# Performance work log

Measured on AMD Instinct MI355X. Metric: run time of the kernel, lower is better.

Reference implementation:

```python
import jax, jax.numpy as jnp
import numpy as np

B, S, E, H = 2, 2048, 2048, 16
D = E // H  # head_dim = 128
ROPE_BASE = 10000.0


def _rope_tables(seq_len, dim, dtype):
    inv_freq = 1.0 / (ROPE_BASE ** (jnp.arange(0, dim, 2, dtype=jnp.float32) / dim))
    pos = jnp.arange(seq_len, dtype=jnp.float32)
    freqs = jnp.outer(pos, inv_freq)            # [S, D/2]
    emb = jnp.concatenate([freqs, freqs], -1)    # [S, D]
    return jnp.cos(emb).astype(dtype), jnp.sin(emb).astype(dtype)


def _rotate_half(x):
    x1, x2 = jnp.split(x, 2, axis=-1)
    return jnp.concatenate([-x2, x1], axis=-1)


def _apply_rope(x, cos, sin):
    # x: [B,H,S,D]; cos/sin: [S,D] broadcast over batch+heads
    return x * cos[None, None] + _rotate_half(x) * sin[None, None]


def setup_inputs() -> dict:
    key = jax.random.key(0)
    k1, k2, k3 = jax.random.split(key, 3)
    x = jax.random.normal(k1, (B, S, E), dtype=jnp.float32)
    w_qkv = jax.random.normal(k2, (3 * E, E), dtype=jnp.float32) * (E ** -0.5)
    w_out = jax.random.normal(k3, (E, E), dtype=jnp.float32) * (E ** -0.5)
    return {"x": x, "w_qkv": w_qkv, "w_out": w_out}


def reference(x, w_qkv, w_out):
    b, s, e = x.shape
    qkv = x @ w_qkv.T                                # [B,S,3E]
    q, k, v = jnp.split(qkv, 3, axis=-1)
    def to_heads(t):
        return t.reshape(b, s, H, D).transpose(0, 2, 1, 3)  # [B,H,S,D]
    q, k, v = to_heads(q), to_heads(k), to_heads(v)
    cos, sin = _rope_tables(s, D, x.dtype)
    q = _apply_rope(q, cos, sin)
    k = _apply_rope(k, cos, sin)
    scale = 1.0 / jnp.sqrt(jnp.asarray(D, x.dtype))
    scores = jnp.einsum('bhqd,bhkd->bhqk', q, k) * scale
    causal = jnp.tril(jnp.ones((s, s), dtype=bool))
    scores = jnp.where(causal[None, None], scores, jnp.asarray(-jnp.inf, scores.dtype))
    attn = jax.nn.softmax(scores, axis=-1)
    y = jnp.einsum('bhqk,bhkd->bhqd', attn, v)       # [B,H,S,D]
    y = y.transpose(0, 2, 1, 3).reshape(b, s, e)
    return y @ w_out.T
```

## Files before the change

kernel.cpp:

```cpp
#include <hip/hip_runtime.h>
#include <stdint.h>

constexpr int BATCH = 2;
constexpr int SEQ   = 2048;
constexpr int EMB   = 2048;
constexpr int NH    = 16;
constexpr int HD    = 128;
constexpr int QKV3  = 3 * EMB;

typedef unsigned short u16;
typedef __attribute__((ext_vector_type(8))) short bf16x8;
typedef __attribute__((ext_vector_type(4))) float floatx4;

__device__ inline float bf2f(u16 u) {
  union { unsigned int i; float f; } v; v.i = ((unsigned int)u) << 16; return v.f;
}
__device__ inline u16 f2bf(float f) {
  union { float f; unsigned int i; } v; v.f = f;
  unsigned int x = v.i;
  return (u16)((x + 0x7fffu + ((x >> 16) & 1u)) >> 16);
}

__device__ inline void load_lds16(const void* g, void* l) {
  __builtin_amdgcn_global_load_lds((const __attribute__((address_space(1))) unsigned int*)g,
                                   (__attribute__((address_space(3))) unsigned int*)l,
                                   16, 0, 0);
}

__device__ inline void block_barrier() {
  __builtin_amdgcn_sched_barrier(0);
  asm volatile("" ::: "memory");
  __builtin_amdgcn_s_barrier();
  asm volatile("" ::: "memory");
  __builtin_amdgcn_sched_barrier(0);
}

__global__ void cvt_f32_bf16(const float* __restrict__ src, u16* __restrict__ dst, int n4) {
  const int i = blockIdx.x * blockDim.x + threadIdx.x;
  if (i < n4) {
    const float4 v = ((const float4*)src)[i];
    ushort4 o;
    o.x = f2bf(v.x); o.y = f2bf(v.y); o.z = f2bf(v.z); o.w = f2bf(v.w);
    ((ushort4*)dst)[i] = o;
  }
}

__global__ __launch_bounds__(512, 2) void gemm_bt192(const u16* __restrict__ A,
                                                     const u16* __restrict__ Bm,
                                                     u16* __restrict__ Cb,
                                                     int M, int N, int K) {
  __shared__ __align__(16) u16 sh[57344];
  char* ldsb = (char*)sh;

  const int tid  = threadIdx.x;
  const int wave = tid >> 6, lane = tid & 63;
  const int wrow = wave >> 1;
  const int wcol = wave & 1;
  const int m0 = blockIdx.y * 256, n0 = blockIdx.x * 192;
  const int frow = lane & 15, quad = lane >> 4;
  const int KT = K >> 6;

  const int srow8 = tid >> 3;
  const int scolE = (((tid & 7) ^ (srow8 & 7)) << 3);
  auto stageT = [&](int t, int d) {
#pragma unroll
    for (int a = 0; a < 4; ++a) {
      const int r = a * 64 + srow8;
      load_lds16(A + (size_t)(m0 + r) * K + t * 64 + scolE,
                 ldsb + d * 57344 + a * 8192 + wave * 1024);
    }
#pragma unroll
    for (int bi = 0; bi < 3; ++bi) {
      const int r = bi * 64 + srow8;
      load_lds16(Bm + (size_t)(n0 + r) * K + t * 64 + scolE,
                 ldsb + d * 57344 + 32768 + bi * 8192 + wave * 1024);
    }
  };

  floatx4 acc[4][6];
#pragma unroll
  for (int i = 0; i < 4; ++i)
#pragma unroll
    for (int j = 0; j < 6; ++j) acc[i][j] = {0.f, 0.f, 0.f, 0.f};

  stageT(0, 0);

  for (int t = 0; t < KT; ++t) {
    const int d = t & 1, dn = d ^ 1;
    const char* dbuf = ldsb + d * 57344;

    block_barrier();
    if (t + 1 < KT) {
      stageT(t + 1, dn);
      asm volatile("s_waitcnt vmcnt(7)" ::: "memory");
    } else {
      asm volatile("s_waitcnt vmcnt(0)" ::: "memory");
    }
    block_barrier();

    bf16x8 af[4][2], bf0[2][2], bf1[2][2], bf2[2][2];
#pragma unroll
    for (int mi = 0; mi < 4; ++mi) {
      const int ra = wrow * 64 + mi * 16 + frow;
#pragma unroll
      for (int kk = 0; kk < 2; ++kk) {
        const int cb = (kk * 64 + quad * 16) ^ ((ra & 7) << 4);
        af[mi][kk] = *(const bf16x8*)(dbuf + ra * 128 + cb);
      }
    }
#pragma unroll
    for (int ni = 0; ni < 2; ++ni) {
      const int rb = wcol * 96 + ni * 16 + frow;
#pragma unroll
      for (int kk = 0; kk < 2; ++kk) {
        const int cb = (kk * 64 + quad * 16) ^ ((rb & 7) << 4);
        bf0[ni][kk] = *(const bf16x8*)(dbuf + 32768 + rb * 128 + cb);
      }
    }
#pragma unroll
    for (int ni = 0; ni < 2; ++ni) {
      const int rb = wcol * 96 + (2 + ni) * 16 + frow;
#pragma unroll
      for (int kk = 0; kk < 2; ++kk) {
        const int cb = (kk * 64 + quad * 16) ^ ((rb & 7) << 4);
        bf1[ni][kk] = *(const bf16x8*)(dbuf + 32768 + rb * 128 + cb);
      }
    }
    asm volatile("s_waitcnt lgkmcnt(4)" ::: "memory");
    __builtin_amdgcn_sched_barrier(0);
    __builtin_amdgcn_s_setprio(1);
#pragma unroll
    for (int mi = 0; mi < 4; ++mi)
#pragma unroll
      for (int ni = 0; ni < 2; ++ni)
#pragma unroll
        for (int kk = 0; kk < 2; ++kk)
          acc[mi][ni] = __builtin_amdgcn_mfma_f32_16x16x32_bf16(af[mi][kk], bf0[ni][kk], acc[mi][ni], 0, 0, 0);
    __builtin_amdgcn_s_setprio(0);

#pragma unroll
    for (int ni = 0; ni < 2; ++ni) {
      const int rb = wcol * 96 + (4 + ni) * 16 + frow;
#pragma unroll
      for (int kk = 0; kk < 2; ++kk) {
        const int cb = (kk * 64 + quad * 16) ^ ((rb & 7) << 4);
        bf2[ni][kk] = *(const bf16x8*)(dbuf + 32768 + rb * 128 + cb);
      }
    }
    asm volatile("s_waitcnt lgkmcnt(4)" ::: "memory");
    __builtin_amdgcn_sched_barrier(0);
    __builtin_amdgcn_s_setprio(1);
#pragma unroll
    for (int mi = 0; mi < 4; ++mi)
#pragma unroll
      for (int ni = 0; ni < 2; ++ni)
#pragma unroll
        for (int kk = 0; kk < 2; ++kk)
          acc[mi][2 + ni] = __builtin_amdgcn_mfma_f32_16x16x32_bf16(af[mi][kk], bf1[ni][kk], acc[mi][2 + ni], 0, 0, 0);
    __builtin_amdgcn_s_setprio(0);

    asm volatile("s_waitcnt lgkmcnt(0)" ::: "memory");
    __builtin_amdgcn_sched_barrier(0);
    __builtin_amdgcn_s_setprio(1);
#pragma unroll
    for (int mi = 0; mi < 4; ++mi)
#pragma unroll
      for (int ni = 0; ni < 2; ++ni)
#pragma unroll
        for (int kk = 0; kk < 2; ++kk)
          acc[mi][4 + ni] = __builtin_amdgcn_mfma_f32_16x16x32_bf16(af[mi][kk], bf2[ni][kk], acc[mi][4 + ni], 0, 0, 0);
    __builtin_amdgcn_s_setprio(0);
  }

#pragma unroll
  for (int mi = 0; mi < 4; ++mi)
#pragma unroll
    for (int ni = 0; ni < 6; ++ni) {
      const int row = m0 + wrow * 64 + mi * 16 + quad * 4;
      const int col = n0 + wcol * 96 + ni * 16 + frow;
#pragma unroll
      for (int r = 0; r < 4; ++r)
        Cb[(size_t)(row + r) * N + col] = f2bf(acc[mi][ni][r]);
    }
}

__global__ __launch_bounds__(512, 2) void gemm_bt128f(const u16* __restrict__ A,
                                                      const u16* __restrict__ Bm,
                                                      float* __restrict__ Cf,
                                                      int M, int N, int K) {
  __shared__ __align__(16) u16 sh[49152];
  char* ldsb = (char*)sh;

  const int tid  = threadIdx.x;
  const int wave = tid >> 6, lane = tid & 63;
  const int wrow = wave >> 1;
  const int wcol = wave & 1;
  const int m0 = blockIdx.y * 256, n0 = blockIdx.x * 128;
  const int frow = lane & 15, quad = lane >> 4;
  const int KT = K >> 6;

  const int srow8 = tid >> 3;
  const int scolE = (((tid & 7) ^ (srow8 & 7)) << 3);
  auto stageT = [&](int t, int d) {
#pragma unroll
    for (int a = 0; a < 4; ++a) {
      const int r = a * 64 + srow8;
      load_lds16(A + (size_t)(m0 + r) * K + t * 64 + scolE,
                 ldsb + d * 49152 + a * 8192 + wave * 1024);
    }
#pragma unroll
    for (int bi = 0; bi < 2; ++bi) {
      const int r = bi * 64 + srow8;
      load_lds16(Bm + (size_t)(n0 + r) * K + t * 64 + scolE,
                 ldsb + d * 49152 + 32768 + bi * 8192 + wave * 1024);
    }
  };

  floatx4 acc[4][4];
#pragma unroll
  for (int i = 0; i < 4; ++i)
#pragma unroll
    for (int j = 0; j < 4; ++j) acc[i][j] = {0.f, 0.f, 0.f, 0.f};

  stageT(0, 0);

  for (int t = 0; t < KT; ++t) {
    const int d = t & 1, dn = d ^ 1;
    const char* dbuf = ldsb + d * 49152;

    block_barrier();
    if (t + 1 < KT) {
      stageT(t + 1, dn);
      asm volatile("s_waitcnt vmcnt(6)" ::: "memory");
    } else {
      asm volatile("s_waitcnt vmcnt(0)" ::: "memory");
    }
    block_barrier();

    bf16x8 af[4][2], bf0[2][2], bf1[2][2];
#pragma unroll
    for (int mi = 0; mi < 4; ++mi) {
      const int ra = wrow * 64 + mi * 16 + frow;
#pragma unroll
      for (int kk = 0; kk < 2; ++kk) {
        const int cb = (kk * 64 + quad * 16) ^ ((ra & 7) << 4);
        af[mi][kk] = *(const bf16x8*)(dbuf + ra * 128 + cb);
      }
    }
#pragma unroll
    for (int ni = 0; ni < 2; ++ni) {
      const int rb = wcol * 64 + ni * 16 + frow;
#pragma unroll
      for (int kk = 0; kk < 2; ++kk) {
        const int cb = (kk * 64 + quad * 16) ^ ((rb & 7) << 4);
        bf0[ni][kk] = *(const bf16x8*)(dbuf + 32768 + rb * 128 + cb);
      }
    }
#pragma unroll
    for (int ni = 0; ni < 2; ++ni) {
      const int rb = wcol * 64 + (2 + ni) * 16 + frow;
#pragma unroll
      for (int kk = 0; kk < 2; ++kk) {
        const int cb = (kk * 64 + quad * 16) ^ ((rb & 7) << 4);
        bf1[ni][kk] = *(const bf16x8*)(dbuf + 32768 + rb * 128 + cb);
      }
    }
    asm volatile("s_waitcnt lgkmcnt(4)" ::: "memory");
    __builtin_amdgcn_sched_barrier(0);
    __builtin_amdgcn_s_setprio(1);
#pragma unroll
    for (int mi = 0; mi < 4; ++mi)
#pragma unroll
      for (int ni = 0; ni < 2; ++ni)
#pragma unroll
        for (int kk = 0; kk < 2; ++kk)
          acc[mi][ni] = __builtin_amdgcn_mfma_f32_16x16x32_bf16(af[mi][kk], bf0[ni][kk], acc[mi][ni], 0, 0, 0);
    __builtin_amdgcn_s_setprio(0);

    asm volatile("s_waitcnt lgkmcnt(0)" ::: "memory");
    __builtin_amdgcn_sched_barrier(0);
    __builtin_amdgcn_s_setprio(1);
#pragma unroll
    for (int mi = 0; mi < 4; ++mi)
#pragma unroll
      for (int ni = 0; ni < 2; ++ni)
#pragma unroll
        for (int kk = 0; kk < 2; ++kk)
          acc[mi][2 + ni] = __builtin_amdgcn_mfma_f32_16x16x32_bf16(af[mi][kk], bf1[ni][kk], acc[mi][2 + ni], 0, 0, 0);
    __builtin_amdgcn_s_setprio(0);
  }

#pragma unroll
  for (int mi = 0; mi < 4; ++mi)
#pragma unroll
    for (int ni = 0; ni < 4; ++ni) {
      const int row = m0 + wrow * 64 + mi * 16 + quad * 4;
      const int col = n0 + wcol * 64 + ni * 16 + frow;
#pragma unroll
      for (int r = 0; r < 4; ++r)
        Cf[(size_t)(row + r) * N + col] = acc[mi][ni][r];
    }
}

__global__ void rope_inplace(u16* __restrict__ qkv) {
  const int t   = blockIdx.x * blockDim.x + threadIdx.x;
  const int j   = t & 63;
  const int idx = t >> 6;
  const int h   = idx & (NH - 1);
  const int bs  = idx >> 4;
  const int s   = bs & (SEQ - 1);

  u16* base = qkv + (size_t)bs * QKV3 + h * HD;

  const float inv_freq = exp2f(-(float)j * (13.287712379549449f / 64.0f));
  const float ang = (float)s * inv_freq;
  const float c = cosf(ang), sn = sinf(ang);

#pragma unroll
  for (int part = 0; part < 2; ++part) {
    u16* p = base + part * EMB;
    const float x1 = bf2f(p[j]), x2 = bf2f(p[j + 64]);
    p[j]      = f2bf(x1 * c - x2 * sn);
    p[j + 64] = f2bf(x2 * c + x1 * sn);
  }
}

__global__ __launch_bounds__(256) void transpose_v(const u16* __restrict__ qkv,
                                                   u16* __restrict__ VT) {
  __shared__ u16 vtile[64][136];
  const int tid = threadIdx.x;
  const int s0 = blockIdx.x * 64;
  const int bh = blockIdx.y;
  const int b = bh >> 4, h = bh & 15;

  const u16* Vp = qkv + (size_t)b * SEQ * QKV3 + 2 * EMB + h * HD;
  {
    const int r = tid >> 2, cp = (tid & 3) * 32;
    const uint4* src = (const uint4*)(Vp + (size_t)(s0 + r) * QKV3 + cp);
    uint4* dst = (uint4*)&vtile[r][cp];
    dst[0] = src[0]; dst[1] = src[1]; dst[2] = src[2]; dst[3] = src[3];
  }
  __syncthreads();
  {
    const int d = tid >> 1, ck = (tid & 1) * 32;
    ushort4 o[8];
#pragma unroll
    for (int i = 0; i < 8; ++i) {
      o[i].x = vtile[ck + i * 4 + 0][d];
      o[i].y = vtile[ck + i * 4 + 1][d];
      o[i].z = vtile[ck + i * 4 + 2][d];
      o[i].w = vtile[ck + i * 4 + 3][d];
    }
    ushort4* dst = (ushort4*)(VT + ((size_t)bh * HD + d) * SEQ + s0 + ck);
#pragma unroll
    for (int i = 0; i < 8; ++i) dst[i] = o[i];
  }
}

constexpr int PSTR = 72;

__global__ __launch_bounds__(256, 2) void attn_mfma(const u16* __restrict__ qkv,
                                                    const u16* __restrict__ VT,
                                                    u16* __restrict__ Y) {
  __shared__ __align__(16) u16 kb[2][64 * 128];
  __shared__ __align__(16) u16 vb[2][64 * 128];
  __shared__ __align__(16) u16 p_sh[4][16][PSTR];

  const int tid  = threadIdx.x;
  const int wave = tid >> 6, lane = tid & 63;
  const int bid  = blockIdx.x;
  const int bh   = bid & 31;
  const int pc   = bid >> 5;
  const int cq   = (pc < 8) ? pc : 23 - pc;
  const int qa   = cq;
  const int qb   = 31 - cq;
  const int b = bh >> 4, h = bh & 15;

  const u16* Qp  = qkv + (size_t)b * SEQ * QKV3 + h * HD;
  const u16* Kp  = Qp + EMB;
  const u16* VTp = VT + (size_t)bh * HD * SEQ;

  const int NT = 32 - cq;

  u16* kbf = &kb[0][0];

  {
    const int rl  = lane >> 4;
    const int cbp = (lane & 15) * 16;
#pragma unroll
    for (int i = 0; i < 8; ++i) {
      const int cc = wave * 8 + i;
      const int r  = cc * 4 + rl;
      const int gq = (r < 64) ? (qa * 64 + r) : (qb * 64 + r - 64);
      const int cbl = cbp ^ ((r & 7) << 4);
      load_lds16(Qp + (size_t)gq * QKV3 + (cbl >> 1), kbf + cc * 512);
    }
  }
  asm volatile("s_waitcnt vmcnt(0)" ::: "memory");
  block_barrier();

  const int frow = lane & 15;
  const int quad = lane >> 4;

  bf16x8 aq[2][4];
#pragma unroll
  for (int m = 0; m < 2; ++m)
#pragma unroll
    for (int ks = 0; ks < 4; ++ks) {
      const int qr = m * 64 + wave * 16 + frow;
      const int cb = (ks * 64 + quad * 16) ^ ((qr & 7) << 4);
      aq[m][ks] = *(const bf16x8*)((const char*)kbf + qr * 256 + cb);
    }
  asm volatile("s_waitcnt lgkmcnt(0)" ::: "memory");
  block_barrier();

  auto stage_k = [&](int t, int sel) {
    const int rl  = lane >> 4;
    const int cbp = (lane & 15) * 16;
#pragma unroll
    for (int i = 0; i < 4; ++i) {
      const int cc = wave * 4 + i;
      const int r  = cc * 4 + rl;
      const int cbl = cbp ^ ((r & 7) << 4);
      load_lds16(Kp + (size_t)(t * 64 + r) * QKV3 + (cbl >> 1), &kb[sel][cc * 512]);
    }
  };
  auto stage_v = [&](int t, int sel) {
    const int rl  = lane >> 3;
    const int cbp = (lane & 7) * 16;
#pragma unroll
    for (int i = 0; i < 4; ++i) {
      const int cc = wave * 4 + i;
      const int r  = cc * 8 + rl;
      const int cbl = cbp ^ ((r & 7) << 4);
      load_lds16(VTp + (size_t)r * SEQ + t * 64 + (cbl >> 1), &vb[sel][cc * 512]);
    }
  };

  floatx4 o_acc[2][8];
#pragma unroll
  for (int m = 0; m < 2; ++m)
#pragma unroll
    for (int dt = 0; dt < 8; ++dt) o_acc[m][dt] = {0.f, 0.f, 0.f, 0.f};
  float l_r[2][4];
#pragma unroll
  for (int m = 0; m < 2; ++m)
#pragma unroll
    for (int r = 0; r < 4; ++r) l_r[m][r] = 0.f;

  const float scale = 0.08838834764831845f;
  const float M0s   = 3.5355339059327378f;

  stage_k(0, 0);
  stage_v(0, 0);

  for (int t = 0; t < NT; ++t) {
    block_barrier();
    const bool havek = (t + 1 < NT);
    if (havek) {
      stage_k(t + 1, (t + 1) & 1);
      stage_v(t + 1, (t + 1) & 1);
      asm volatile("s_waitcnt vmcnt(8)" ::: "memory");
    } else {
      asm volatile("s_waitcnt vmcnt(0)" ::: "memory");
    }
    block_barrier();

    const char* kbuf = (const char*)&kb[t & 1][0];
    const char* vbuf = (const char*)&vb[t & 1][0];
    const bool aAct = (t <= qa);

    floatx4 s4[2][4];
    __builtin_amdgcn_s_setprio(1);
    if (aAct) {
#pragma unroll
      for (int nt = 0; nt < 4; ++nt) {
        floatx4 a0 = {0.f, 0.f, 0.f, 0.f}, a1 = {0.f, 0.f, 0.f, 0.f};
#pragma unroll
        for (int ks = 0; ks < 4; ++ks) {
          const int kr = nt * 16 + frow;
          const int cb = (ks * 64 + quad * 16) ^ ((kr & 7) << 4);
          const bf16x8 bk = *(const bf16x8*)(kbuf + kr * 256 + cb);
          a0 = __builtin_amdgcn_mfma_f32_16x16x32_bf16(aq[0][ks], bk, a0, 0, 0, 0);
          a1 = __builtin_amdgcn_mfma_f32_16x16x32_bf16(aq[1][ks], bk, a1, 0, 0, 0);
        }
        s4[0][nt] = a0; s4[1][nt] = a1;
      }
    } else {
#pragma unroll
      for (int nt = 0; nt < 4; ++nt) {
        floatx4 a1 = {0.f, 0.f, 0.f, 0.f};
#pragma unroll
        for (int ks = 0; ks < 4; ++ks) {
          const int kr = nt * 16 + frow;
          const int cb = (ks * 64 + quad * 16) ^ ((kr & 7) << 4);
          const bf16x8 bk = *(const bf16x8*)(kbuf + kr * 256 + cb);
          a1 = __builtin_amdgcn_mfma_f32_16x16x32_bf16(aq[1][ks], bk, a1, 0, 0, 0);
        }
        s4[1][nt] = a1;
      }
    }
    __builtin_amdgcn_s_setprio(0);

#pragma unroll
    for (int m = 0; m < 2; ++m) {
      if (m == 0 && !aAct) continue;
      const int tdiag = (m == 0) ? qa : qb;
      if (t == tdiag) {
#pragma unroll
        for (int nt = 0; nt < 4; ++nt)
#pragma unroll
          for (int r = 0; r < 4; ++r) {
            const int key = t * 64 + nt * 16 + frow;
            const int qg  = tdiag * 64 + wave * 16 + quad * 4 + r;
            if (key > qg) s4[m][nt][r] = -1.0e30f;
          }
      }
#pragma unroll
      for (int nt = 0; nt < 4; ++nt)
#pragma unroll
        for (int r = 0; r < 4; ++r)
          s4[m][nt][r] = __expf(fmaf(s4[m][nt][r], scale, -M0s));
#pragma unroll
      for (int r = 0; r < 4; ++r)
        l_r[m][r] += (s4[m][0][r] + s4[m][1][r]) + (s4[m][2][r] + s4[m][3][r]);
    }

    __builtin_amdgcn_s_setprio(1);
#pragma unroll
    for (int m = 0; m < 2; ++m) {
      if (m == 0 && !aAct) continue;
#pragma unroll
      for (int nt = 0; nt < 4; ++nt)
#pragma unroll
        for (int r = 0; r < 4; ++r)
          p_sh[wave][quad * 4 + r][nt * 16 + frow] = f2bf(s4[m][nt][r]);
#pragma unroll
      for (int step = 0; step < 2; ++step) {
        const bf16x8 ap = *(const bf16x8*)&p_sh[wave][frow][step * 32 + quad * 8];
#pragma unroll
        for (int dt = 0; dt < 8; ++dt) {
          const int vr = dt * 16 + frow;
          const int cb = (step * 64 + quad * 16) ^ ((vr & 7) << 4);
          const bf16x8 bv = *(const bf16x8*)(vbuf + vr * 128 + cb);
          o_acc[m][dt] = __builtin_amdgcn_mfma_f32_16x16x32_bf16(ap, bv, o_acc[m][dt], 0, 0, 0);
        }
      }
    }
    __builtin_amdgcn_s_setprio(0);
  }

#pragma unroll
  for (int off = 1; off <= 8; off <<= 1)
#pragma unroll
    for (int m = 0; m < 2; ++m)
#pragma unroll
      for (int r = 0; r < 4; ++r) l_r[m][r] += __shfl_xor(l_r[m][r], off);

#pragma unroll
  for (int m = 0; m < 2; ++m) {
    const int qbase = ((m == 0) ? qa : qb) * 64 + wave * 16;
    float invl[4];
#pragma unroll
    for (int r = 0; r < 4; ++r) invl[r] = 1.f / l_r[m][r];
#pragma unroll
    for (int dt = 0; dt < 8; ++dt)
#pragma unroll
      for (int r = 0; r < 4; ++r) {
        const int qg = qbase + quad * 4 + r;
        const size_t off = ((size_t)b * SEQ + qg) * EMB + h * HD + dt * 16 + frow;
        Y[off] = f2bf(o_acc[m][dt][r] * invl[r]);
      }
  }
}

extern "C" void kernel_launch(void* const* d_in, const int* in_sizes, int n_in,
                              void* d_out, int out_size, void* d_ws, size_t ws_size,
                              hipStream_t stream) {
  const float* x_f     = (const float*)d_in[0];
  const float* w_qkv_f = (const float*)d_in[1];
  const float* w_out_f = (const float*)d_in[2];
  float* out = (float*)d_out;

  const int M = BATCH * SEQ;
  const size_t n_x    = (size_t)M * EMB;
  const size_t n_wqkv = (size_t)3 * EMB * EMB;
  const size_t n_wout = (size_t)EMB * EMB;

  u16* xb    = (u16*)d_ws;
  u16* wqkvb = xb + n_x;
  u16* qkv   = wqkvb + n_wqkv;
  u16* VT    = qkv + (size_t)M * QKV3;
  u16* woutb = wqkvb;
  u16* Yb    = xb;

  cvt_f32_bf16<<<(int)((n_x / 4 + 255) / 256), 256, 0, stream>>>(x_f, xb, (int)(n_x / 4));
  cvt_f32_bf16<<<(int)((n_wqkv / 4 + 255) / 256), 256, 0, stream>>>(w_qkv_f, wqkvb, (int)(n_wqkv / 4));

  gemm_bt192<<<dim3(QKV3 / 192, M / 256), 512, 0, stream>>>(
      xb, wqkvb, qkv, M, QKV3, EMB);

  rope_inplace<<<(BATCH * SEQ * NH * 64) / 256, 256, 0, stream>>>(qkv);
  transpose_v<<<dim3(SEQ / 64, BATCH * NH), 256, 0, stream>>>(qkv, VT);

  cvt_f32_bf16<<<(int)((n_wout / 4 + 255) / 256), 256, 0, stream>>>(w_out_f, woutb, (int)(n_wout / 4));

  attn_mfma<<<dim3((SEQ / 128) * BATCH * NH), 256, 0, stream>>>(qkv, VT, Yb);

  gemm_bt128f<<<dim3(EMB / 128, M / 256), 512, 0, stream>>>(
      Yb, woutb, out, M, EMB, EMB);
}
```

Baseline: 362.9 us.

## Interleave global-to-LDS prefetch chunks with MFMA phases in both GEMM kernels

Restructures the main loop of both GEMM kernels so the next tile's global-to-LDS loads are issued in small chunks spread across several MFMA phases, instead of all at once at the top of the iteration. The 192-wide kernel now computes in four 2x3 sub-block quadrants with extra block barriers between them. The goal is to spread memory traffic across the iteration and overlap it with compute. In exchange it adds many block barriers per iteration and a full vmcnt(0) wait at the top of each iteration, which could serialize the waves.

Measured after the change: 357.2 us. No clear change (-1.6%).

```diff
diff --git a/kernel.cpp b/kernel.cpp
--- a/kernel.cpp
+++ b/kernel.cpp
@@ -62,15 +62,13 @@
 
   const int srow8 = tid >> 3;
   const int scolE = (((tid & 7) ^ (srow8 & 7)) << 3);
-  auto stageT = [&](int t, int d) {
-#pragma unroll
-    for (int a = 0; a < 4; ++a) {
-      const int r = a * 64 + srow8;
+  auto stage1 = [&](int t, int d, int j) {
+    if (j < 4) {
+      const int r = j * 64 + srow8;
       load_lds16(A + (size_t)(m0 + r) * K + t * 64 + scolE,
-                 ldsb + d * 57344 + a * 8192 + wave * 1024);
-    }
-#pragma unroll
-    for (int bi = 0; bi < 3; ++bi) {
+                 ldsb + d * 57344 + j * 8192 + wave * 1024);
+    } else {
+      const int bi = j - 4;
       const int r = bi * 64 + srow8;
       load_lds16(Bm + (size_t)(n0 + r) * K + t * 64 + scolE,
                  ldsb + d * 57344 + 32768 + bi * 8192 + wave * 1024);
@@ -83,93 +81,101 @@
 #pragma unroll
     for (int j = 0; j < 6; ++j) acc[i][j] = {0.f, 0.f, 0.f, 0.f};
 
-  stageT(0, 0);
+#pragma unroll
+  for (int j = 0; j < 7; ++j) stage1(0, 0, j);
+
+  auto rdA = [&](const char* dbuf, int mi, int kk) -> bf16x8 {
+    const int ra = wrow * 64 + mi * 16 + frow;
+    const int cb = (kk * 64 + quad * 16) ^ ((ra & 7) << 4);
+    return *(const bf16x8*)(dbuf + ra * 128 + cb);
+  };
+  auto rdB = [&](const char* dbuf, int ni, int kk) -> bf16x8 {
+    const int rb = wcol * 96 + ni * 16 + frow;
+    const int cb = (kk * 64 + quad * 16) ^ ((rb & 7) << 4);
+    return *(const bf16x8*)(dbuf + 32768 + rb * 128 + cb);
+  };
 
   for (int t = 0; t < KT; ++t) {
     const int d = t & 1, dn = d ^ 1;
     const char* dbuf = ldsb + d * 57344;
-
-    block_barrier();
-    if (t + 1 < KT) {
-      stageT(t + 1, dn);
-      asm volatile("s_waitcnt vmcnt(7)" ::: "memory");
-    } else {
-      asm volatile("s_waitcnt vmcnt(0)" ::: "memory");
-    }
-    block_barrier();
-
-    bf16x8 af[4][2], bf0[2][2], bf1[2][2], bf2[2][2];
-#pragma unroll
-    for (int mi = 0; mi < 4; ++mi) {
-      const int ra = wrow * 64 + mi * 16 + frow;
-#pragma unroll
-      for (int kk = 0; kk < 2; ++kk) {
-        const int cb = (kk * 64 + quad * 16) ^ ((ra & 7) << 4);
-        af[mi][kk] = *(const bf16x8*)(dbuf + ra * 128 + cb);
-      }
-    }
-#pragma unroll
-    for (int ni = 0; ni < 2; ++ni) {
-      const int rb = wcol * 96 + ni * 16 + frow;
-#pragma unroll
-      for (int kk = 0; kk < 2; ++kk) {
-        const int cb = (kk * 64 + quad * 16) ^ ((rb & 7) << 4);
-        bf0[ni][kk] = *(const bf16x8*)(dbuf + 32768 + rb * 128 + cb);
-      }
-    }
-#pragma unroll
-    for (int ni = 0; ni < 2; ++ni) {
-      const int rb = wcol * 96 + (2 + ni) * 16 + frow;
-#pragma unroll
-      for (int kk = 0; kk < 2; ++kk) {
-        const int cb = (kk * 64 + quad * 16) ^ ((rb & 7) << 4);
-        bf1[ni][kk] = *(const bf16x8*)(dbuf + 32768 + rb * 128 + cb);
-      }
-    }
-    asm volatile("s_waitcnt lgkmcnt(4)" ::: "memory");
-    __builtin_amdgcn_sched_barrier(0);
-    __builtin_amdgcn_s_setprio(1);
-#pragma unroll
-    for (int mi = 0; mi < 4; ++mi)
-#pragma unroll
-      for (int ni = 0; ni < 2; ++ni)
-#pragma unroll
-        for (int kk = 0; kk < 2; ++kk)
-          acc[mi][ni] = __builtin_amdgcn_mfma_f32_16x16x32_bf16(af[mi][kk], bf0[ni][kk], acc[mi][ni], 0, 0, 0);
-    __builtin_amdgcn_s_setprio(0);
-
-#pragma unroll
-    for (int ni = 0; ni < 2; ++ni) {
-      const int rb = wcol * 96 + (4 + ni) * 16 + frow;
-#pragma unroll
-      for (int kk = 0; kk < 2; ++kk) {
-        const int cb = (kk * 64 + quad * 16) ^ ((rb & 7) << 4);
-        bf2[ni][kk] = *(const bf16x8*)(dbuf + 32768 + rb * 128 + cb);
-      }
-    }
-    asm volatile("s_waitcnt lgkmcnt(4)" ::: "memory");
-    __builtin_amdgcn_sched_barrier(0);
-    __builtin_amdgcn_s_setprio(1);
-#pragma unroll
-    for (int mi = 0; mi < 4; ++mi)
-#pragma unroll
-      for (int ni = 0; ni < 2; ++ni)
-#pragma unroll
-        for (int kk = 0; kk < 2; ++kk)
-          acc[mi][2 + ni] = __builtin_amdgcn_mfma_f32_16x16x32_bf16(af[mi][kk], bf1[ni][kk], acc[mi][2 + ni], 0, 0, 0);
-    __builtin_amdgcn_s_setprio(0);
-
+    const bool pf = (t + 1 < KT);
+
+    asm volatile("s_waitcnt vmcnt(0)" ::: "memory");
+    block_barrier();
+
+    bf16x8 a0[2][2], a1[2][2], b0[3][2], b1[3][2];
+
+#pragma unroll
+    for (int mi = 0; mi < 2; ++mi)
+#pragma unroll
+      for (int kk = 0; kk < 2; ++kk) a0[mi][kk] = rdA(dbuf, mi, kk);
+#pragma unroll
+    for (int ni = 0; ni < 3; ++ni)
+#pragma unroll
+      for (int kk = 0; kk < 2; ++kk) b0[ni][kk] = rdB(dbuf, ni, kk);
+    if (pf) { stage1(t + 1, dn, 0); stage1(t + 1, dn, 1); stage1(t + 1, dn, 2); }
+    block_barrier();
     asm volatile("s_waitcnt lgkmcnt(0)" ::: "memory");
     __builtin_amdgcn_sched_barrier(0);
     __builtin_amdgcn_s_setprio(1);
 #pragma unroll
-    for (int mi = 0; mi < 4; ++mi)
-#pragma unroll
-      for (int ni = 0; ni < 2; ++ni)
+    for (int mi = 0; mi < 2; ++mi)
+#pragma unroll
+      for (int ni = 0; ni < 3; ++ni)
 #pragma unroll
         for (int kk = 0; kk < 2; ++kk)
-          acc[mi][4 + ni] = __builtin_amdgcn_mfma_f32_16x16x32_bf16(af[mi][kk], bf2[ni][kk], acc[mi][4 + ni], 0, 0, 0);
-    __builtin_amdgcn_s_setprio(0);
+          acc[mi][ni] = __builtin_amdgcn_mfma_f32_16x16x32_bf16(a0[mi][kk], b0[ni][kk], acc[mi][ni], 0, 0, 0);
+    __builtin_amdgcn_s_setprio(0);
+    block_barrier();
+
+#pragma unroll
+    for (int mi = 0; mi < 2; ++mi)
+#pragma unroll
+      for (int kk = 0; kk < 2; ++kk) a1[mi][kk] = rdA(dbuf, 2 + mi, kk);
+    if (pf) { stage1(t + 1, dn, 3); stage1(t + 1, dn, 4); }
+    block_barrier();
+    asm volatile("s_waitcnt lgkmcnt(0)" ::: "memory");
+    __builtin_amdgcn_sched_barrier(0);
+    __builtin_amdgcn_s_setprio(1);
+#pragma unroll
+    for (int mi = 0; mi < 2; ++mi)
+#pragma unroll
+      for (int ni = 0; ni < 3; ++ni)
+#pragma unroll
+        for (int kk = 0; kk < 2; ++kk)
+          acc[2 + mi][ni] = __builtin_amdgcn_mfma_f32_16x16x32_bf16(a1[mi][kk], b0[ni][kk], acc[2 + mi][ni], 0, 0, 0);
+    __builtin_amdgcn_s_setprio(0);
+    block_barrier();
+
+#pragma unroll
+    for (int ni = 0; ni < 3; ++ni)
+#pragma unroll
+      for (int kk = 0; kk < 2; ++kk) b1[ni][kk] = rdB(dbuf, 3 + ni, kk);
+    if (pf) { stage1(t + 1, dn, 5); stage1(t + 1, dn, 6); }
+    block_barrier();
+    asm volatile("s_waitcnt lgkmcnt(0)" ::: "memory");
+    __builtin_amdgcn_sched_barrier(0);
+    __builtin_amdgcn_s_setprio(1);
+#pragma unroll
+    for (int mi = 0; mi < 2; ++mi)
+#pragma unroll
+      for (int ni = 0; ni < 3; ++ni)
+#pragma unroll
+        for (int kk = 0; kk < 2; ++kk)
+          acc[2 + mi][3 + ni] = __builtin_amdgcn_mfma_f32_16x16x32_bf16(a1[mi][kk], b1[ni][kk], acc[2 + mi][3 + ni], 0, 0, 0);
+    __builtin_amdgcn_s_setprio(0);
+    block_barrier();
+
+    __builtin_amdgcn_s_setprio(1);
+#pragma unroll
+    for (int mi = 0; mi < 2; ++mi)
+#pragma unroll
+      for (int ni = 0; ni < 3; ++ni)
+#pragma unroll
+        for (int kk = 0; kk < 2; ++kk)
+          acc[mi][3 + ni] = __builtin_amdgcn_mfma_f32_16x16x32_bf16(a0[mi][kk], b1[ni][kk], acc[mi][3 + ni], 0, 0, 0);
+    __builtin_amdgcn_s_setprio(0);
+    block_barrier();
   }
 
 #pragma unroll
@@ -201,15 +207,13 @@
 
   const int srow8 = tid >> 3;
   const int scolE = (((tid & 7) ^ (srow8 & 7)) << 3);
-  auto stageT = [&](int t, int d) {
-#pragma unroll
-    for (int a = 0; a < 4; ++a) {
-      const int r = a * 64 + srow8;
+  auto stage1 = [&](int t, int d, int j) {
+    if (j < 4) {
+      const int r = j * 64 + srow8;
       load_lds16(A + (size_t)(m0 + r) * K + t * 64 + scolE,
-                 ldsb + d * 49152 + a * 8192 + wave * 1024);
-    }
-#pragma unroll
-    for (int bi = 0; bi < 2; ++bi) {
+                 ldsb + d * 49152 + j * 8192 + wave * 1024);
+    } else {
+      const int bi = j - 4;
       const int r = bi * 64 + srow8;
       load_lds16(Bm + (size_t)(n0 + r) * K + t * 64 + scolE,
                  ldsb + d * 49152 + 32768 + bi * 8192 + wave * 1024);
@@ -222,61 +226,40 @@
 #pragma unroll
     for (int j = 0; j < 4; ++j) acc[i][j] = {0.f, 0.f, 0.f, 0.f};
 
-  stageT(0, 0);
+#pragma unroll
+  for (int j = 0; j < 6; ++j) stage1(0, 0, j);
+
+  auto rdA = [&](const char* dbuf, int mi, int kk) -> bf16x8 {
+    const int ra = wrow * 64 + mi * 16 + frow;
+    const int cb = (kk * 64 + quad * 16) ^ ((ra & 7) << 4);
+    return *(const bf16x8*)(dbuf + ra * 128 + cb);
+  };
+  auto rdB = [&](const char* dbuf, int ni, int kk) -> bf16x8 {
+    const int rb = wcol * 64 + ni * 16 + frow;
+    const int cb = (kk * 64 + quad * 16) ^ ((rb & 7) << 4);
+    return *(const bf16x8*)(dbuf + 32768 + rb * 128 + cb);
+  };
 
   for (int t = 0; t < KT; ++t) {
     const int d = t & 1, dn = d ^ 1;
     const char* dbuf = ldsb + d * 49152;
-
-    block_barrier();
-    if (t + 1 < KT) {
-      stageT(t + 1, dn);
-      asm volatile("s_waitcnt vmcnt(6)" ::: "memory");
-    } else {
-      asm volatile("s_waitcnt vmcnt(0)" ::: "memory");
-    }
-    block_barrier();
-
-    bf16x8 af[4][2], bf0[2][2], bf1[2][2];
-#pragma unroll
-    for (int mi = 0; mi < 4; ++mi) {
-      const int ra = wrow * 64 + mi * 16 + frow;
-#pragma unroll
-      for (int kk = 0; kk < 2; ++kk) {
-        const int cb = (kk * 64 + quad * 16) ^ ((ra & 7) << 4);
-        af[mi][kk] = *(const bf16x8*)(dbuf + ra * 128 + cb);
-      }
-    }
-#pragma unroll
-    for (int ni = 0; ni < 2; ++ni) {
-      const int rb = wcol * 64 + ni * 16 + frow;
-#pragma unroll
-      for (int kk = 0; kk < 2; ++kk) {
-        const int cb = (kk * 64 + quad * 16) ^ ((rb & 7) << 4);
-        bf0[ni][kk] = *(const bf16x8*)(dbuf + 32768 + rb * 128 + cb);
-      }
-    }
-#pragma unroll
-    for (int ni = 0; ni < 2; ++ni) {
-      const int rb = wcol * 64 + (2 + ni) * 16 + frow;
-#pragma unroll
-      for (int kk = 0; kk < 2; ++kk) {
-        const int cb = (kk * 64 + quad * 16) ^ ((rb & 7) << 4);
-        bf1[ni][kk] = *(const bf16x8*)(dbuf + 32768 + rb * 128 + cb);
-      }
-    }
-    asm volatile("s_waitcnt lgkmcnt(4)" ::: "memory");
-    __builtin_amdgcn_sched_barrier(0);
-    __builtin_amdgcn_s_setprio(1);
+    const bool pf = (t + 1 < KT);
+
+    asm volatile("s_waitcnt vmcnt(0)" ::: "memory");
+    block_barrier();
+
+    bf16x8 af[4][2], b0[2][2], b1[2][2];
+
 #pragma unroll
     for (int mi = 0; mi < 4; ++mi)
 #pragma unroll
-      for (int ni = 0; ni < 2; ++ni)
-#pragma unroll
-        for (int kk = 0; kk < 2; ++kk)
-          acc[mi][ni] = __builtin_amdgcn_mfma_f32_16x16x32_bf16(af[mi][kk], bf0[ni][kk], acc[mi][ni], 0, 0, 0);
-    __builtin_amdgcn_s_setprio(0);
-
+      for (int kk = 0; kk < 2; ++kk) af[mi][kk] = rdA(dbuf, mi, kk);
+#pragma unroll
+    for (int ni = 0; ni < 2; ++ni)
+#pragma unroll
+      for (int kk = 0; kk < 2; ++kk) b0[ni][kk] = rdB(dbuf, ni, kk);
+    if (pf) { stage1(t + 1, dn, 0); stage1(t + 1, dn, 1); stage1(t + 1, dn, 2); }
+    block_barrier();
     asm volatile("s_waitcnt lgkmcnt(0)" ::: "memory");
     __builtin_amdgcn_sched_barrier(0);
     __builtin_amdgcn_s_setprio(1);
@@ -286,8 +269,28 @@
       for (int ni = 0; ni < 2; ++ni)
 #pragma unroll
         for (int kk = 0; kk < 2; ++kk)
-          acc[mi][2 + ni] = __builtin_amdgcn_mfma_f32_16x16x32_bf16(af[mi][kk], bf1[ni][kk], acc[mi][2 + ni], 0, 0, 0);
-    __builtin_amdgcn_s_setprio(0);
+          acc[mi][ni] = __builtin_amdgcn_mfma_f32_16x16x32_bf16(af[mi][kk], b0[ni][kk], acc[mi][ni], 0, 0, 0);
+    __builtin_amdgcn_s_setprio(0);
+    block_barrier();
+
+#pragma unroll
+    for (int ni = 0; ni < 2; ++ni)
+#pragma unroll
+      for (int kk = 0; kk < 2; ++kk) b1[ni][kk] = rdB(dbuf, 2 + ni, kk);
+    if (pf) { stage1(t + 1, dn, 3); stage1(t + 1, dn, 4); stage1(t + 1, dn, 5); }
+    block_barrier();
+    asm volatile("s_waitcnt lgkmcnt(0)" ::: "memory");
+    __builtin_amdgcn_sched_barrier(0);
+    __builtin_amdgcn_s_setprio(1);
+#pragma unroll
+    for (int mi = 0; mi < 4; ++mi)
+#pragma unroll
+      for (int ni = 0; ni < 2; ++ni)
+#pragma unroll
+        for (int kk = 0; kk < 2; ++kk)
+          acc[mi][2 + ni] = __builtin_amdgcn_mfma_f32_16x16x32_bf16(af[mi][kk], b1[ni][kk], acc[mi][2 + ni], 0, 0, 0);
+    __builtin_amdgcn_s_setprio(0);
+    block_barrier();
   }
 
 #pragma unroll
```
